# Kernel tuning notes

Hardware: AMD Instinct MI355X
Metric: run time of the kernel (lower is better)

## Reference

```python
import jax, jax.numpy as jnp
import numpy as np

B, S, D, H = 2, 2048, 1024, 16
DK = D // H

def setup_inputs() -> dict:
    key = jax.random.key(0)
    ks = jax.random.split(key, 8)
    inp = {
        "Q": jax.random.normal(ks[0], (B, S, D), dtype=jnp.float32),
        "K": jax.random.normal(ks[1], (B, S, D), dtype=jnp.float32),
        "V": jax.random.normal(ks[2], (B, S, D), dtype=jnp.float32),
        "mask": jax.random.randint(ks[3], (B, 1, S, S), 0, 2, dtype=jnp.int32),
        # nn.Linear weights, shape [out_features, in_features], no bias
        "Wq": jax.random.normal(ks[4], (D, D), dtype=jnp.float32) / np.sqrt(D),
        "Wk": jax.random.normal(ks[5], (D, D), dtype=jnp.float32) / np.sqrt(D),
        "Wv": jax.random.normal(ks[6], (D, D), dtype=jnp.float32) / np.sqrt(D),
        "Wo": jax.random.normal(ks[7], (D, D), dtype=jnp.float32) / np.sqrt(D),
    }
    return inp

def reference(Q, K, V, mask, Wq, Wk, Wv, Wo):
    b, s, d = Q.shape
    # projections: y = x @ W.T (torch nn.Linear convention)
    q = (Q @ Wq.T).reshape(b, s, H, DK).transpose(0, 2, 1, 3)  # [b,h,s,dk]
    k = (K @ Wk.T).reshape(b, -1, H, DK).transpose(0, 2, 1, 3)
    v = (V @ Wv.T).reshape(b, -1, H, DK).transpose(0, 2, 1, 3)
    score = jnp.einsum("bhqd,bhkd->bhqk", q, k) / jnp.sqrt(jnp.float32(DK))
    # faithful to source: masked positions get value 1e-9 BEFORE softmax
    score = jnp.where(mask == 0, jnp.float32(1e-9), score)
    attn = jax.nn.softmax(score, axis=-1)
    # dropout p=0.1 treated as eval-mode identity
    out = jnp.einsum("bhqk,bhkd->bhqd", attn, v)  # [b,h,s,dk]
    out = out.transpose(0, 2, 1, 3).reshape(b, s, d)
    return out @ Wo.T
```

## Files before the change

kernel.cpp:

```cpp
#include <hip/hip_runtime.h>

typedef unsigned short u16;
typedef unsigned char  u8;
typedef unsigned long long u64;
typedef __attribute__((ext_vector_type(8))) short bf16x8;
typedef __attribute__((ext_vector_type(4))) float f32x4;

constexpr int B_  = 2;
constexpr int S_  = 2048;
constexpr int D_  = 1024;
constexpr int H_  = 16;
constexpr int DK_ = 64;
constexpr int NROW = B_ * S_;
constexpr size_t QSZ  = (size_t)B_ * H_ * S_ * DK_;
constexpr size_t XBSZ = (size_t)NROW * D_;
constexpr size_t WBSZ = (size_t)D_ * D_;
constexpr size_t MSZ  = (size_t)B_ * S_ * S_;
constexpr size_t MPKB = MSZ / 8;

__device__ __forceinline__ u16 f2bf(float f) {
    union { float f; unsigned u; } c; c.f = f;
    unsigned r = c.u + 0x7fffu + ((c.u >> 16) & 1u);
    return (u16)(r >> 16);
}
__device__ __forceinline__ unsigned pack2(float a, float b) {
    return (unsigned)f2bf(a) | ((unsigned)f2bf(b) << 16);
}
__device__ __forceinline__ unsigned cvt_pk_bf16(float a, float b) {
    unsigned r;
    asm("v_cvt_pk_bf16_f32 %0, %1, %2" : "=v"(r) : "v"(a), "v"(b));
    return r;
}

__device__ __forceinline__ void gl_lds16(const u16* g, u16* l) {
    __builtin_amdgcn_global_load_lds(
        (const __attribute__((address_space(1))) void*)g,
        (__attribute__((address_space(3))) void*)l, 16, 0, 0);
}

__global__ __launch_bounds__(256)
void cvt7m(const float* __restrict__ s0, const float* __restrict__ s1,
           const float* __restrict__ s2, const float* __restrict__ s3,
           const float* __restrict__ s4, const float* __restrict__ s5,
           const float* __restrict__ s6, const int* __restrict__ mk,
           u16* __restrict__ d0, u16* __restrict__ d1, u16* __restrict__ d2,
           u16* __restrict__ d3, u16* __restrict__ d4, u16* __restrict__ d5,
           u16* __restrict__ d6, u8* __restrict__ mp)
{
    constexpr size_t XT = 3 * XBSZ;
    constexpr int NCF = (int)((3 * XBSZ + 4 * WBSZ) / 2048);
    constexpr int NCM = (int)(MSZ / 2048);

    for (int c = blockIdx.x; c < NCF + NCM; c += gridDim.x) {
        if (c < NCF) {
            const size_t base = (size_t)c * 2048;
            const float* s; u16* d; size_t off;
            if (base < XT) {
                const int a = (int)(base >> 22);
                off = base & (XBSZ - 1);
                s = (a == 0) ? s0 : (a == 1) ? s1 : s2;
                d = (a == 0) ? d0 : (a == 1) ? d1 : d2;
            } else {
                const size_t r = base - XT;
                const int a = (int)(r >> 20);
                off = r & (WBSZ - 1);
                s = (a == 0) ? s3 : (a == 1) ? s4 : (a == 2) ? s5 : s6;
                d = (a == 0) ? d3 : (a == 1) ? d4 : (a == 2) ? d5 : d6;
            }
            const size_t e = off + (size_t)threadIdx.x * 8;
            const float4 x0 = *(const float4*)(s + e);
            const float4 x1 = *(const float4*)(s + e + 4);
            uint4 p;
            p.x = pack2(x0.x, x0.y); p.y = pack2(x0.z, x0.w);
            p.z = pack2(x1.x, x1.y); p.w = pack2(x1.z, x1.w);
            *(uint4*)(d + e) = p;
        } else {
            const size_t e = (size_t)(c - NCF) * 2048 + (size_t)threadIdx.x * 8;
            const int4 x0 = *(const int4*)(mk + e);
            const int4 x1 = *(const int4*)(mk + e + 4);
            unsigned bv = (unsigned)(x0.x != 0)        | ((unsigned)(x0.y != 0) << 1)
                        | ((unsigned)(x0.z != 0) << 2) | ((unsigned)(x0.w != 0) << 3)
                        | ((unsigned)(x1.x != 0) << 4) | ((unsigned)(x1.y != 0) << 5)
                        | ((unsigned)(x1.z != 0) << 6) | ((unsigned)(x1.w != 0) << 7);
            mp[e >> 3] = (u8)bv;
        }
    }
}

__global__ __launch_bounds__(256, 3)
void qkv_gemm(const u16* __restrict__ Xq, const u16* __restrict__ Xk,
              const u16* __restrict__ Xv,
              const u16* __restrict__ Wq, const u16* __restrict__ Wk,
              const u16* __restrict__ Wv,
              u16* __restrict__ Yq, u16* __restrict__ Yk, u16* __restrict__ Yv)
{
    __shared__ u16 As[2 * 128 * 32];
    __shared__ u16 Bs[2 * 128 * 32];

    const int z = blockIdx.z;
    const u16* X = (z == 0) ? Xq : (z == 1) ? Xk : Xv;
    const u16* W = (z == 0) ? Wq : (z == 1) ? Wk : Wv;
    u16*       Y = (z == 0) ? Yq : (z == 1) ? Yk : Yv;
    const float osc = (z == 0) ? 0.125f : 1.0f;

    const int tid  = threadIdx.x;
    const int lane = tid & 63;
    const int w    = tid >> 6;
    const int quad = lane >> 4;
    const int lq   = lane & 15;
    const int wm   = (w & 1) << 6;
    const int wn   = (w >> 1) << 6;

    const int m0 = blockIdx.x << 7;
    const int n0 = blockIdx.y << 7;

    const int srow = tid >> 2;
    const int scol = (tid & 3) << 3;
    const u16* ga0 = X + (size_t)(m0 + srow) * D_ + scol;
    const u16* ga1 = ga0 + (size_t)64 * D_;
    const u16* gb0 = W + (size_t)(n0 + srow) * D_ + scol;
    const u16* gb1 = gb0 + (size_t)64 * D_;

    u16* la0 = As + (size_t)w * 512;
    u16* la1 = As + 2048 + (size_t)w * 512;
    u16* lb0 = Bs + (size_t)w * 512;
    u16* lb1 = Bs + 2048 + (size_t)w * 512;

    f32x4 acc[4][4];
#pragma unroll
    for (int i = 0; i < 4; ++i)
#pragma unroll
        for (int j = 0; j < 4; ++j) acc[i][j] = (f32x4){0.f, 0.f, 0.f, 0.f};

    for (int kt = 0; kt < D_; kt += 64) {
        __syncthreads();
        gl_lds16(ga0 + kt, la0);
        gl_lds16(ga1 + kt, la1);
        gl_lds16(gb0 + kt, lb0);
        gl_lds16(gb1 + kt, lb1);
        gl_lds16(ga0 + kt + 32, la0 + 4096);
        gl_lds16(ga1 + kt + 32, la1 + 4096);
        gl_lds16(gb0 + kt + 32, lb0 + 4096);
        gl_lds16(gb1 + kt + 32, lb1 + 4096);
        __syncthreads();

#pragma unroll
        for (int kk = 0; kk < 2; ++kk) {
            bf16x8 af[4], bf[4];
#pragma unroll
            for (int t = 0; t < 4; ++t) {
                af[t] = *(const bf16x8*)&As[(kk << 12) + (size_t)(wm + (t << 4) + lq) * 32 + (quad << 3)];
                bf[t] = *(const bf16x8*)&Bs[(kk << 12) + (size_t)(wn + (t << 4) + lq) * 32 + (quad << 3)];
            }
#pragma unroll
            for (int i = 0; i < 4; ++i)
#pragma unroll
                for (int j = 0; j < 4; ++j)
                    acc[i][j] = __builtin_amdgcn_mfma_f32_16x16x32_bf16(
                        af[i], bf[j], acc[i][j], 0, 0, 0);
        }
    }

#pragma unroll
    for (int i = 0; i < 4; ++i)
#pragma unroll
        for (int j = 0; j < 4; ++j)
#pragma unroll
            for (int r = 0; r < 4; ++r) {
                const int grow = m0 + wm + (i << 4) + (quad << 2) + r;
                const int of   = n0 + wn + (j << 4) + lq;
                const int b = grow >> 11, s = grow & (S_ - 1);
                const int h = of >> 6,    dk = of & 63;
                Y[(((size_t)(b * H_ + h)) * S_ + s) * DK_ + dk] =
                    f2bf(acc[i][j][r] * osc);
            }
}

__global__ __launch_bounds__(256, 4)
void out_gemm(const u16* __restrict__ X, const u16* __restrict__ W,
              float* __restrict__ Y)
{
    __shared__ u16 As[2 * 64 * 32];
    __shared__ u16 Bs[2 * 64 * 32];

    const int tid  = threadIdx.x;
    const int lane = tid & 63;
    const int w    = tid >> 6;
    const int quad = lane >> 4;
    const int lq   = lane & 15;
    const int wm   = (w & 1) << 5;
    const int wn   = (w >> 1) << 5;

    const int m0 = blockIdx.x << 6;
    const int n0 = blockIdx.y << 6;

    const int srow = tid >> 2;
    const int scol = (tid & 3) << 3;
    const u16* ga0 = X + (size_t)(m0 + srow) * D_ + scol;
    const u16* gb0 = W + (size_t)(n0 + srow) * D_ + scol;

    u16* la0 = As + (size_t)w * 512;
    u16* lb0 = Bs + (size_t)w * 512;

    f32x4 acc[2][2];
#pragma unroll
    for (int i = 0; i < 2; ++i)
#pragma unroll
        for (int j = 0; j < 2; ++j) acc[i][j] = (f32x4){0.f, 0.f, 0.f, 0.f};

    for (int kt = 0; kt < D_; kt += 64) {
        __syncthreads();
        gl_lds16(ga0 + kt, la0);
        gl_lds16(gb0 + kt, lb0);
        gl_lds16(ga0 + kt + 32, la0 + 2048);
        gl_lds16(gb0 + kt + 32, lb0 + 2048);
        __syncthreads();

#pragma unroll
        for (int kk = 0; kk < 2; ++kk) {
            bf16x8 af[2], bf[2];
#pragma unroll
            for (int t = 0; t < 2; ++t) {
                af[t] = *(const bf16x8*)&As[(kk << 11) + (size_t)(wm + (t << 4) + lq) * 32 + (quad << 3)];
                bf[t] = *(const bf16x8*)&Bs[(kk << 11) + (size_t)(wn + (t << 4) + lq) * 32 + (quad << 3)];
            }
#pragma unroll
            for (int i = 0; i < 2; ++i)
#pragma unroll
                for (int j = 0; j < 2; ++j)
                    acc[i][j] = __builtin_amdgcn_mfma_f32_16x16x32_bf16(
                        af[i], bf[j], acc[i][j], 0, 0, 0);
        }
    }

#pragma unroll
    for (int i = 0; i < 2; ++i)
#pragma unroll
        for (int j = 0; j < 2; ++j)
#pragma unroll
            for (int r = 0; r < 4; ++r) {
                const int grow = m0 + wm + (i << 4) + (quad << 2) + r;
                const int gcol = n0 + wn + (j << 4) + lq;
                Y[(size_t)grow * D_ + gcol] = acc[i][j][r];
            }
}

constexpr int AP = 72;

__global__ __launch_bounds__(256, 2)
void attn_mfma8(const u16* __restrict__ qb, const u16* __restrict__ kb,
                const u16* __restrict__ vb, const u8* __restrict__ mpk,
                u16* __restrict__ ctx)
{
    __shared__ u16 Qs[128][AP];
    __shared__ u16 Ks[64][AP];
    __shared__ u16 Vt[64][AP];
    __shared__ u16 Ps[128][AP];

    const int tid  = threadIdx.x;
    const int lane = tid & 63;
    const int w    = tid >> 6;
    const int quad = lane >> 4;
    const int lq   = lane & 15;
    const int w32  = w << 5;

    const int bid = (int)(blockIdx.x + gridDim.x * (blockIdx.y + gridDim.y * blockIdx.z));
    const int swz = (bid & 7) * 64 + (bid >> 3);
    const int q0 = (swz & 15) << 7;
    const int h  = (swz >> 4) & 15;
    const int b  = swz >> 8;

    const u16* qbh = qb + (((size_t)b * H_ + h) * S_ + q0) * DK_;
    const u16* kbh = kb + ((size_t)b * H_ + h) * S_ * DK_;
    const u16* vbh = vb + ((size_t)b * H_ + h) * S_ * DK_;

    {
        const int r = tid >> 1, c = (tid & 1) << 5;
#pragma unroll
        for (int u = 0; u < 4; ++u)
            *(uint4*)&Qs[r][c + (u << 3)] =
                *(const uint4*)&qbh[(size_t)r * DK_ + c + (u << 3)];
    }
    __syncthreads();
    bf16x8 aQ[2][2];
#pragma unroll
    for (int i = 0; i < 2; ++i) {
        aQ[i][0] = *(const bf16x8*)&Qs[w32 + (i << 4) + lq][quad << 3];
        aQ[i][1] = *(const bf16x8*)&Qs[w32 + (i << 4) + lq][32 + (quad << 3)];
    }

    f32x4 O[2][4];
    float lsum[2][4];
#pragma unroll
    for (int i = 0; i < 2; ++i)
#pragma unroll
        for (int t = 0; t < 4; ++t) O[i][t] = (f32x4){0.f, 0.f, 0.f, 0.f};
#pragma unroll
    for (int i = 0; i < 2; ++i)
#pragma unroll
        for (int r = 0; r < 4; ++r) lsum[i][r] = 0.f;

    const int ksr = tid >> 2, ksc = (tid & 3) << 4;
    const int vc  = tid & 15;
    const int vs  = (tid >> 4) & 1;
    const int vk0 = vc + (vs << 5);
    const int vdg = tid >> 5;
    const int vcol = (vc << 2) + (vs << 1);

    uint4 kr0, kr1, vr0, vr1;
    {
        kr0 = *(const uint4*)&kbh[(size_t)ksr * DK_ + ksc];
        kr1 = *(const uint4*)&kbh[(size_t)ksr * DK_ + ksc + 8];
        vr0 = *(const uint4*)&vbh[(size_t)vk0 * DK_ + (vdg << 3)];
        vr1 = *(const uint4*)&vbh[(size_t)(vk0 + 16) * DK_ + (vdg << 3)];
    }

    const int qrow0 = q0 + w32 + (quad << 2);
    const u8* mrow = mpk + (size_t)b * S_ * (S_ / 8) + (size_t)qrow0 * (S_ / 8);

    for (int k0 = 0; k0 < S_; k0 += 64) {
        u64 mw[2][4];
#pragma unroll
        for (int i = 0; i < 2; ++i)
#pragma unroll
            for (int r = 0; r < 4; ++r)
                mw[i][r] = *(const u64*)&mrow[(size_t)((i << 4) + r) * (S_ / 8) + (k0 >> 3)];

        __syncthreads();
        {
            *(uint4*)&Ks[ksr][ksc]     = kr0;
            *(uint4*)&Ks[ksr][ksc + 8] = kr1;
            const u16* a0 = (const u16*)&vr0;
            const u16* a1 = (const u16*)&vr1;
#pragma unroll
            for (int i = 0; i < 8; ++i)
                *(ushort2*)&Vt[(vdg << 3) + i][vcol] = (ushort2){a0[i], a1[i]};
        }
        __syncthreads();

        if (k0 + 64 < S_) {
            const size_t kb0 = (size_t)(k0 + 64 + ksr) * DK_ + ksc;
            kr0 = *(const uint4*)&kbh[kb0];
            kr1 = *(const uint4*)&kbh[kb0 + 8];
            const size_t vb0 = (size_t)(k0 + 64 + vk0) * DK_ + (vdg << 3);
            vr0 = *(const uint4*)&vbh[vb0];
            vr1 = *(const uint4*)&vbh[vb0 + (size_t)16 * DK_];
        }

        f32x4 st[2][4];
#pragma unroll
        for (int t = 0; t < 4; ++t) {
            const bf16x8 b0 = *(const bf16x8*)&Ks[(t << 4) + lq][quad << 3];
            const bf16x8 b1 = *(const bf16x8*)&Ks[(t << 4) + lq][32 + (quad << 3)];
#pragma unroll
            for (int i = 0; i < 2; ++i) {
                f32x4 c = {0.f, 0.f, 0.f, 0.f};
                c = __builtin_amdgcn_mfma_f32_16x16x32_bf16(aQ[i][0], b0, c, 0, 0, 0);
                c = __builtin_amdgcn_mfma_f32_16x16x32_bf16(aQ[i][1], b1, c, 0, 0, 0);
                st[i][t] = c;
            }
        }

#pragma unroll
        for (int i = 0; i < 2; ++i)
#pragma unroll
            for (int r = 0; r < 4; ++r) {
                const unsigned lo = (unsigned)mw[i][r];
                const unsigned hi = (unsigned)(mw[i][r] >> 32);
                float p0 = __expf(st[i][0][r]);
                float p1 = __expf(st[i][1][r]);
                float p2 = __expf(st[i][2][r]);
                float p3 = __expf(st[i][3][r]);
                p0 = ((lo >> lq) & 1u) ? p0 : 1.0f;
                p1 = ((lo >> (lq + 16)) & 1u) ? p1 : 1.0f;
                p2 = ((hi >> lq) & 1u) ? p2 : 1.0f;
                p3 = ((hi >> (lq + 16)) & 1u) ? p3 : 1.0f;
                lsum[i][r] += (p0 + p1) + (p2 + p3);
                uint2 pw;
                pw.x = cvt_pk_bf16(p0, p1);
                pw.y = cvt_pk_bf16(p2, p3);
                *(uint2*)&Ps[w32 + (i << 4) + (quad << 2) + r][lq << 2] = pw;
            }

        bf16x8 aP[2][2];
#pragma unroll
        for (int i = 0; i < 2; ++i) {
            aP[i][0] = *(const bf16x8*)&Ps[w32 + (i << 4) + lq][quad << 3];
            aP[i][1] = *(const bf16x8*)&Ps[w32 + (i << 4) + lq][32 + (quad << 3)];
        }
#pragma unroll
        for (int t = 0; t < 4; ++t) {
            const bf16x8 b0 = *(const bf16x8*)&Vt[(t << 4) + lq][quad << 3];
            const bf16x8 b1 = *(const bf16x8*)&Vt[(t << 4) + lq][32 + (quad << 3)];
#pragma unroll
            for (int i = 0; i < 2; ++i) {
                O[i][t] = __builtin_amdgcn_mfma_f32_16x16x32_bf16(aP[i][0], b0, O[i][t], 0, 0, 0);
                O[i][t] = __builtin_amdgcn_mfma_f32_16x16x32_bf16(aP[i][1], b1, O[i][t], 0, 0, 0);
            }
        }
    }

#pragma unroll
    for (int i = 0; i < 2; ++i)
#pragma unroll
        for (int r = 0; r < 4; ++r) {
#pragma unroll
            for (int off = 1; off < 16; off <<= 1)
                lsum[i][r] += __shfl_xor(lsum[i][r], off);
            lsum[i][r] = 1.0f / lsum[i][r];
        }

#pragma unroll
    for (int i = 0; i < 2; ++i)
#pragma unroll
        for (int t = 0; t < 4; ++t)
#pragma unroll
            for (int r = 0; r < 4; ++r) {
                const int row = qrow0 + (i << 4) + r;
                ctx[((size_t)b * S_ + row) * D_ + (h << 6) + (t << 4) + lq] =
                    f2bf(O[i][t][r] * lsum[i][r]);
            }
}

extern "C" void kernel_launch(void* const* d_in, const int* in_sizes, int n_in,
                              void* d_out, int out_size, void* d_ws, size_t ws_size,
                              hipStream_t stream)
{
    const float* Q    = (const float*)d_in[0];
    const float* K    = (const float*)d_in[1];
    const float* V    = (const float*)d_in[2];
    const int*   mask = (const int*)d_in[3];
    const float* Wq   = (const float*)d_in[4];
    const float* Wk   = (const float*)d_in[5];
    const float* Wv   = (const float*)d_in[6];
    const float* Wo   = (const float*)d_in[7];
    float* out = (float*)d_out;

    u16* xqb = (u16*)d_ws;
    u16* xkb = xqb + XBSZ;
    u16* xvb = xqb + 2 * XBSZ;
    u16* wqb = xqb + 3 * XBSZ;
    u16* wkb = wqb + WBSZ;
    u16* wvb = wqb + 2 * WBSZ;
    u16* wob = wqb + 3 * WBSZ;
    u16* qw  = wqb + 4 * WBSZ;
    u16* kw  = qw + QSZ;
    u16* vw  = qw + 2 * QSZ;
    u8*  mpk = (u8*)(qw + 3 * QSZ);
    u16* cx  = xqb;

    hipLaunchKernelGGL(cvt7m, dim3(2048), dim3(256), 0, stream,
                       Q, K, V, Wq, Wk, Wv, Wo, mask,
                       xqb, xkb, xvb, wqb, wkb, wvb, wob, mpk);
    hipLaunchKernelGGL(qkv_gemm, dim3(NROW / 128, D_ / 128, 3), dim3(256), 0, stream,
                       xqb, xkb, xvb, wqb, wkb, wvb, qw, kw, vw);
    hipLaunchKernelGGL(attn_mfma8, dim3(S_ / 128, H_, B_), dim3(256), 0, stream,
                       qw, kw, vw, mpk, cx);
    hipLaunchKernelGGL(out_gemm, dim3(NROW / 64, D_ / 64), dim3(256), 0, stream,
                       cx, wob, out);
}
```

Measured before the change: 252.0 us.

## Split attention block across 8 waves with warp-specialized K/V staging

```diff
diff --git a/kernel.cpp b/kernel.cpp
--- a/kernel.cpp
+++ b/kernel.cpp
@@ -247,22 +247,21 @@
 
 constexpr int AP = 72;
 
-__global__ __launch_bounds__(256, 2)
-void attn_mfma8(const u16* __restrict__ qb, const u16* __restrict__ kb,
+__global__ __launch_bounds__(512, 4)
+void attn_mfma9(const u16* __restrict__ qb, const u16* __restrict__ kb,
                 const u16* __restrict__ vb, const u8* __restrict__ mpk,
                 u16* __restrict__ ctx)
 {
-    __shared__ u16 Qs[128][AP];
-    __shared__ u16 Ks[64][AP];
-    __shared__ u16 Vt[64][AP];
-    __shared__ u16 Ps[128][AP];
+    __shared__ __align__(16) u16 Ks[64][AP];
+    __shared__ __align__(16) u16 Vt[64][AP];
+    __shared__ __align__(16) u16 Ps[128][AP];
 
     const int tid  = threadIdx.x;
     const int lane = tid & 63;
     const int w    = tid >> 6;
     const int quad = lane >> 4;
     const int lq   = lane & 15;
-    const int w32  = w << 5;
+    const int w16  = w << 4;
 
     const int bid = (int)(blockIdx.x + gridDim.x * (blockIdx.y + gridDim.y * blockIdx.z));
     const int swz = (bid & 7) * 64 + (bid >> 3);
@@ -274,62 +273,51 @@
     const u16* kbh = kb + ((size_t)b * H_ + h) * S_ * DK_;
     const u16* vbh = vb + ((size_t)b * H_ + h) * S_ * DK_;
 
+    bf16x8 aQ0, aQ1;
     {
-        const int r = tid >> 1, c = (tid & 1) << 5;
-#pragma unroll
-        for (int u = 0; u < 4; ++u)
-            *(uint4*)&Qs[r][c + (u << 3)] =
-                *(const uint4*)&qbh[(size_t)r * DK_ + c + (u << 3)];
-    }
-    __syncthreads();
-    bf16x8 aQ[2][2];
-#pragma unroll
-    for (int i = 0; i < 2; ++i) {
-        aQ[i][0] = *(const bf16x8*)&Qs[w32 + (i << 4) + lq][quad << 3];
-        aQ[i][1] = *(const bf16x8*)&Qs[w32 + (i << 4) + lq][32 + (quad << 3)];
-    }
-
-    f32x4 O[2][4];
-    float lsum[2][4];
-#pragma unroll
-    for (int i = 0; i < 2; ++i)
-#pragma unroll
-        for (int t = 0; t < 4; ++t) O[i][t] = (f32x4){0.f, 0.f, 0.f, 0.f};
-#pragma unroll
-    for (int i = 0; i < 2; ++i)
-#pragma unroll
-        for (int r = 0; r < 4; ++r) lsum[i][r] = 0.f;
+        const size_t qr = (size_t)(w16 + lq) * DK_;
+        aQ0 = *(const bf16x8*)&qbh[qr + (quad << 3)];
+        aQ1 = *(const bf16x8*)&qbh[qr + 32 + (quad << 3)];
+    }
+
+    f32x4 O[4];
+    float lsum[4];
+#pragma unroll
+    for (int t = 0; t < 4; ++t) O[t] = (f32x4){0.f, 0.f, 0.f, 0.f};
+#pragma unroll
+    for (int r = 0; r < 4; ++r) lsum[r] = 0.f;
 
     const int ksr = tid >> 2, ksc = (tid & 3) << 4;
-    const int vc  = tid & 15;
-    const int vs  = (tid >> 4) & 1;
+    const int t2  = tid - 256;
+    const int vc  = t2 & 15;
+    const int vs  = (t2 >> 4) & 1;
     const int vk0 = vc + (vs << 5);
-    const int vdg = tid >> 5;
+    const int vdg = t2 >> 5;
     const int vcol = (vc << 2) + (vs << 1);
 
     uint4 kr0, kr1, vr0, vr1;
-    {
+    if (w < 4) {
         kr0 = *(const uint4*)&kbh[(size_t)ksr * DK_ + ksc];
         kr1 = *(const uint4*)&kbh[(size_t)ksr * DK_ + ksc + 8];
+    } else {
         vr0 = *(const uint4*)&vbh[(size_t)vk0 * DK_ + (vdg << 3)];
         vr1 = *(const uint4*)&vbh[(size_t)(vk0 + 16) * DK_ + (vdg << 3)];
     }
 
-    const int qrow0 = q0 + w32 + (quad << 2);
+    const int qrow0 = q0 + w16 + (quad << 2);
     const u8* mrow = mpk + (size_t)b * S_ * (S_ / 8) + (size_t)qrow0 * (S_ / 8);
 
+    u64 mw[4], mwn[4];
+#pragma unroll
+    for (int r = 0; r < 4; ++r)
+        mw[r] = *(const u64*)&mrow[(size_t)r * (S_ / 8)];
+
     for (int k0 = 0; k0 < S_; k0 += 64) {
-        u64 mw[2][4];
-#pragma unroll
-        for (int i = 0; i < 2; ++i)
-#pragma unroll
-            for (int r = 0; r < 4; ++r)
-                mw[i][r] = *(const u64*)&mrow[(size_t)((i << 4) + r) * (S_ / 8) + (k0 >> 3)];
-
-        __syncthreads();
-        {
+        __syncthreads();
+        if (w < 4) {
             *(uint4*)&Ks[ksr][ksc]     = kr0;
             *(uint4*)&Ks[ksr][ksc + 8] = kr1;
+        } else {
             const u16* a0 = (const u16*)&vr0;
             const u16* a1 = (const u16*)&vr1;
 #pragma unroll
@@ -339,87 +327,87 @@
         __syncthreads();
 
         if (k0 + 64 < S_) {
-            const size_t kb0 = (size_t)(k0 + 64 + ksr) * DK_ + ksc;
-            kr0 = *(const uint4*)&kbh[kb0];
-            kr1 = *(const uint4*)&kbh[kb0 + 8];
-            const size_t vb0 = (size_t)(k0 + 64 + vk0) * DK_ + (vdg << 3);
-            vr0 = *(const uint4*)&vbh[vb0];
-            vr1 = *(const uint4*)&vbh[vb0 + (size_t)16 * DK_];
-        }
-
-        f32x4 st[2][4];
+            if (w < 4) {
+                const size_t kb0 = (size_t)(k0 + 64 + ksr) * DK_ + ksc;
+                kr0 = *(const uint4*)&kbh[kb0];
+                kr1 = *(const uint4*)&kbh[kb0 + 8];
+            } else {
+                const size_t vb0 = (size_t)(k0 + 64 + vk0) * DK_ + (vdg << 3);
+                vr0 = *(const uint4*)&vbh[vb0];
+                vr1 = *(const uint4*)&vbh[vb0 + (size_t)16 * DK_];
+            }
+#pragma unroll
+            for (int r = 0; r < 4; ++r)
+                mwn[r] = *(const u64*)&mrow[(size_t)r * (S_ / 8) + ((k0 + 64) >> 3)];
+        }
+
+        f32x4 st[4];
+        __builtin_amdgcn_s_setprio(1);
 #pragma unroll
         for (int t = 0; t < 4; ++t) {
             const bf16x8 b0 = *(const bf16x8*)&Ks[(t << 4) + lq][quad << 3];
             const bf16x8 b1 = *(const bf16x8*)&Ks[(t << 4) + lq][32 + (quad << 3)];
-#pragma unroll
-            for (int i = 0; i < 2; ++i) {
-                f32x4 c = {0.f, 0.f, 0.f, 0.f};
-                c = __builtin_amdgcn_mfma_f32_16x16x32_bf16(aQ[i][0], b0, c, 0, 0, 0);
-                c = __builtin_amdgcn_mfma_f32_16x16x32_bf16(aQ[i][1], b1, c, 0, 0, 0);
-                st[i][t] = c;
-            }
-        }
-
-#pragma unroll
-        for (int i = 0; i < 2; ++i)
-#pragma unroll
-            for (int r = 0; r < 4; ++r) {
-                const unsigned lo = (unsigned)mw[i][r];
-                const unsigned hi = (unsigned)(mw[i][r] >> 32);
-                float p0 = __expf(st[i][0][r]);
-                float p1 = __expf(st[i][1][r]);
-                float p2 = __expf(st[i][2][r]);
-                float p3 = __expf(st[i][3][r]);
-                p0 = ((lo >> lq) & 1u) ? p0 : 1.0f;
-                p1 = ((lo >> (lq + 16)) & 1u) ? p1 : 1.0f;
-                p2 = ((hi >> lq) & 1u) ? p2 : 1.0f;
-                p3 = ((hi >> (lq + 16)) & 1u) ? p3 : 1.0f;
-                lsum[i][r] += (p0 + p1) + (p2 + p3);
-                uint2 pw;
-                pw.x = cvt_pk_bf16(p0, p1);
-                pw.y = cvt_pk_bf16(p2, p3);
-                *(uint2*)&Ps[w32 + (i << 4) + (quad << 2) + r][lq << 2] = pw;
-            }
-
-        bf16x8 aP[2][2];
-#pragma unroll
-        for (int i = 0; i < 2; ++i) {
-            aP[i][0] = *(const bf16x8*)&Ps[w32 + (i << 4) + lq][quad << 3];
-            aP[i][1] = *(const bf16x8*)&Ps[w32 + (i << 4) + lq][32 + (quad << 3)];
-        }
+            f32x4 c = {0.f, 0.f, 0.f, 0.f};
+            c = __builtin_amdgcn_mfma_f32_16x16x32_bf16(aQ0, b0, c, 0, 0, 0);
+            c = __builtin_amdgcn_mfma_f32_16x16x32_bf16(aQ1, b1, c, 0, 0, 0);
+            st[t] = c;
+        }
+        __builtin_amdgcn_s_setprio(0);
+
+#pragma unroll
+        for (int r = 0; r < 4; ++r) {
+            const unsigned lo = (unsigned)mw[r];
+            const unsigned hi = (unsigned)(mw[r] >> 32);
+            float p0 = __expf(st[0][r]);
+            float p1 = __expf(st[1][r]);
+            float p2 = __expf(st[2][r]);
+            float p3 = __expf(st[3][r]);
+            p0 = ((lo >> lq) & 1u) ? p0 : 1.0f;
+            p1 = ((lo >> (lq + 16)) & 1u) ? p1 : 1.0f;
+            p2 = ((hi >> lq) & 1u) ? p2 : 1.0f;
+            p3 = ((hi >> (lq + 16)) & 1u) ? p3 : 1.0f;
+            lsum[r] += (p0 + p1) + (p2 + p3);
+            uint2 pw;
+            pw.x = cvt_pk_bf16(p0, p1);
+            pw.y = cvt_pk_bf16(p2, p3);
+            *(uint2*)&Ps[w16 + (quad << 2) + r][lq << 2] = pw;
+        }
+
+        bf16x8 aP0, aP1;
+        aP0 = *(const bf16x8*)&Ps[w16 + lq][quad << 3];
+        aP1 = *(const bf16x8*)&Ps[w16 + lq][32 + (quad << 3)];
+        __builtin_amdgcn_s_setprio(1);
 #pragma unroll
         for (int t = 0; t < 4; ++t) {
             const bf16x8 b0 = *(const bf16x8*)&Vt[(t << 4) + lq][quad << 3];
             const bf16x8 b1 = *(const bf16x8*)&Vt[(t << 4) + lq][32 + (quad << 3)];
-#pragma unroll
-            for (int i = 0; i < 2; ++i) {
-                O[i][t] = __builtin_amdgcn_mfma_f32_16x16x32_bf16(aP[i][0], b0, O[i][t], 0, 0, 0);
-                O[i][t] = __builtin_amdgcn_mfma_f32_16x16x32_bf16(aP[i][1], b1, O[i][t], 0, 0, 0);
-            }
-        }
-    }
-
-#pragma unroll
-    for (int i = 0; i < 2; ++i)
+            O[t] = __builtin_amdgcn_mfma_f32_16x16x32_bf16(aP0, b0, O[t], 0, 0, 0);
+            O[t] = __builtin_amdgcn_mfma_f32_16x16x32_bf16(aP1, b1, O[t], 0, 0, 0);
+        }
+        __builtin_amdgcn_s_setprio(0);
+
+        if (k0 + 64 < S_) {
+#pragma unroll
+            for (int r = 0; r < 4; ++r) mw[r] = mwn[r];
+        }
+    }
+
+#pragma unroll
+    for (int r = 0; r < 4; ++r) {
+#pragma unroll
+        for (int off = 1; off < 16; off <<= 1)
+            lsum[r] += __shfl_xor(lsum[r], off);
+        lsum[r] = 1.0f / lsum[r];
+    }
+
+#pragma unroll
+    for (int t = 0; t < 4; ++t)
 #pragma unroll
         for (int r = 0; r < 4; ++r) {
-#pragma unroll
-            for (int off = 1; off < 16; off <<= 1)
-                lsum[i][r] += __shfl_xor(lsum[i][r], off);
-            lsum[i][r] = 1.0f / lsum[i][r];
-        }
-
-#pragma unroll
-    for (int i = 0; i < 2; ++i)
-#pragma unroll
-        for (int t = 0; t < 4; ++t)
-#pragma unroll
-            for (int r = 0; r < 4; ++r) {
-                const int row = qrow0 + (i << 4) + r;
-                ctx[((size_t)b * S_ + row) * D_ + (h << 6) + (t << 4) + lq] =
-                    f2bf(O[i][t][r] * lsum[i][r]);
-            }
+            const int row = qrow0 + r;
+            ctx[((size_t)b * S_ + row) * D_ + (h << 6) + (t << 4) + lq] =
+                f2bf(O[t][r] * lsum[r]);
+        }
 }
 
 extern "C" void kernel_launch(void* const* d_in, const int* in_sizes, int n_in,
@@ -454,7 +442,7 @@
                        xqb, xkb, xvb, wqb, wkb, wvb, wob, mpk);
     hipLaunchKernelGGL(qkv_gemm, dim3(NROW / 128, D_ / 128, 3), dim3(256), 0, stream,
                        xqb, xkb, xvb, wqb, wkb, wvb, qw, kw, vw);
-    hipLaunchKernelGGL(attn_mfma8, dim3(S_ / 128, H_, B_), dim3(256), 0, stream,
+    hipLaunchKernelGGL(attn_mfma9, dim3(S_ / 128, H_, B_), dim3(512), 0, stream,
                        qw, kw, vw, mpk, cx);
     hipLaunchKernelGGL(out_gemm, dim3(NROW / 64, D_ / 64), dim3(256), 0, stream,
                        cx, wob, out);
```

New measurement: 253.0 us. Within noise of the previous version (+0.4%).

## Split attention key range in two and combine partial outputs in separate kernel

Applied to the files above, without the earlier changes.

```diff
diff --git a/kernel.cpp b/kernel.cpp
--- a/kernel.cpp
+++ b/kernel.cpp
@@ -17,6 +17,7 @@
 constexpr size_t WBSZ = (size_t)D_ * D_;
 constexpr size_t MSZ  = (size_t)B_ * S_ * S_;
 constexpr size_t MPKB = MSZ / 8;
+constexpr size_t NRH  = (size_t)B_ * H_ * S_;
 
 __device__ __forceinline__ u16 f2bf(float f) {
     union { float f; unsigned u; } c; c.f = f;
@@ -247,15 +248,15 @@
 
 constexpr int AP = 72;
 
-__global__ __launch_bounds__(256, 2)
-void attn_mfma8(const u16* __restrict__ qb, const u16* __restrict__ kb,
-                const u16* __restrict__ vb, const u8* __restrict__ mpk,
-                u16* __restrict__ ctx)
+__global__ __launch_bounds__(256, 4)
+void attn_mfma10(const u16* __restrict__ qb, const u16* __restrict__ kb,
+                 const u16* __restrict__ vb, const u8* __restrict__ mpk,
+                 float* __restrict__ opA, float* __restrict__ opB,
+                 float* __restrict__ lsA, float* __restrict__ lsB)
 {
-    __shared__ u16 Qs[128][AP];
-    __shared__ u16 Ks[64][AP];
-    __shared__ u16 Vt[64][AP];
-    __shared__ u16 Ps[128][AP];
+    __shared__ __align__(16) u16 Ks[64][AP];
+    __shared__ __align__(16) u16 Vt[64][AP];
+    __shared__ __align__(16) u16 Ps[128][AP];
 
     const int tid  = threadIdx.x;
     const int lane = tid & 63;
@@ -265,28 +266,22 @@
     const int w32  = w << 5;
 
     const int bid = (int)(blockIdx.x + gridDim.x * (blockIdx.y + gridDim.y * blockIdx.z));
-    const int swz = (bid & 7) * 64 + (bid >> 3);
-    const int q0 = (swz & 15) << 7;
-    const int h  = (swz >> 4) & 15;
-    const int b  = swz >> 8;
+    const int swz = (bid & 7) * 128 + (bid >> 3);
+    const int ks = swz & 1;
+    const int q0 = ((swz >> 1) & 15) << 7;
+    const int h  = (swz >> 5) & 15;
+    const int b  = swz >> 9;
 
     const u16* qbh = qb + (((size_t)b * H_ + h) * S_ + q0) * DK_;
-    const u16* kbh = kb + ((size_t)b * H_ + h) * S_ * DK_;
-    const u16* vbh = vb + ((size_t)b * H_ + h) * S_ * DK_;
-
-    {
-        const int r = tid >> 1, c = (tid & 1) << 5;
-#pragma unroll
-        for (int u = 0; u < 4; ++u)
-            *(uint4*)&Qs[r][c + (u << 3)] =
-                *(const uint4*)&qbh[(size_t)r * DK_ + c + (u << 3)];
-    }
-    __syncthreads();
+    const u16* kbh = kb + (((size_t)b * H_ + h) * S_ + (ks << 10)) * DK_;
+    const u16* vbh = vb + (((size_t)b * H_ + h) * S_ + (ks << 10)) * DK_;
+
     bf16x8 aQ[2][2];
 #pragma unroll
     for (int i = 0; i < 2; ++i) {
-        aQ[i][0] = *(const bf16x8*)&Qs[w32 + (i << 4) + lq][quad << 3];
-        aQ[i][1] = *(const bf16x8*)&Qs[w32 + (i << 4) + lq][32 + (quad << 3)];
+        const size_t qr = (size_t)(w32 + (i << 4) + lq) * DK_;
+        aQ[i][0] = *(const bf16x8*)&qbh[qr + (quad << 3)];
+        aQ[i][1] = *(const bf16x8*)&qbh[qr + 32 + (quad << 3)];
     }
 
     f32x4 O[2][4];
@@ -316,9 +311,10 @@
     }
 
     const int qrow0 = q0 + w32 + (quad << 2);
-    const u8* mrow = mpk + (size_t)b * S_ * (S_ / 8) + (size_t)qrow0 * (S_ / 8);
-
-    for (int k0 = 0; k0 < S_; k0 += 64) {
+    const u8* mrow = mpk + (size_t)b * S_ * (S_ / 8) + (size_t)qrow0 * (S_ / 8)
+                   + (ks << 7);
+
+    for (int k0 = 0; k0 < 1024; k0 += 64) {
         u64 mw[2][4];
 #pragma unroll
         for (int i = 0; i < 2; ++i)
@@ -338,7 +334,7 @@
         }
         __syncthreads();
 
-        if (k0 + 64 < S_) {
+        if (k0 + 64 < 1024) {
             const size_t kb0 = (size_t)(k0 + 64 + ksr) * DK_ + ksc;
             kr0 = *(const uint4*)&kbh[kb0];
             kr1 = *(const uint4*)&kbh[kb0 + 8];
@@ -348,6 +344,7 @@
         }
 
         f32x4 st[2][4];
+        __builtin_amdgcn_s_setprio(1);
 #pragma unroll
         for (int t = 0; t < 4; ++t) {
             const bf16x8 b0 = *(const bf16x8*)&Ks[(t << 4) + lq][quad << 3];
@@ -360,6 +357,7 @@
                 st[i][t] = c;
             }
         }
+        __builtin_amdgcn_s_setprio(0);
 
 #pragma unroll
         for (int i = 0; i < 2; ++i)
@@ -388,6 +386,7 @@
             aP[i][0] = *(const bf16x8*)&Ps[w32 + (i << 4) + lq][quad << 3];
             aP[i][1] = *(const bf16x8*)&Ps[w32 + (i << 4) + lq][32 + (quad << 3)];
         }
+        __builtin_amdgcn_s_setprio(1);
 #pragma unroll
         for (int t = 0; t < 4; ++t) {
             const bf16x8 b0 = *(const bf16x8*)&Vt[(t << 4) + lq][quad << 3];
@@ -398,6 +397,7 @@
                 O[i][t] = __builtin_amdgcn_mfma_f32_16x16x32_bf16(aP[i][1], b1, O[i][t], 0, 0, 0);
             }
         }
+        __builtin_amdgcn_s_setprio(0);
     }
 
 #pragma unroll
@@ -407,9 +407,11 @@
 #pragma unroll
             for (int off = 1; off < 16; off <<= 1)
                 lsum[i][r] += __shfl_xor(lsum[i][r], off);
-            lsum[i][r] = 1.0f / lsum[i][r];
-        }
-
+        }
+
+    float* op = ks ? opB : opA;
+    float* ls = ks ? lsB : lsA;
+    const size_t rbase = ((size_t)b * H_ + h) * S_;
 #pragma unroll
     for (int i = 0; i < 2; ++i)
 #pragma unroll
@@ -417,9 +419,44 @@
 #pragma unroll
             for (int r = 0; r < 4; ++r) {
                 const int row = qrow0 + (i << 4) + r;
-                ctx[((size_t)b * S_ + row) * D_ + (h << 6) + (t << 4) + lq] =
-                    f2bf(O[i][t][r] * lsum[i][r]);
-            }
+                op[(rbase + row) * DK_ + (t << 4) + lq] = O[i][t][r];
+            }
+    if (lq == 0) {
+#pragma unroll
+        for (int i = 0; i < 2; ++i)
+#pragma unroll
+            for (int r = 0; r < 4; ++r)
+                ls[rbase + qrow0 + (i << 4) + r] = lsum[i][r];
+    }
+}
+
+__global__ __launch_bounds__(256)
+void combine2(const float* __restrict__ opA, const float* __restrict__ opB,
+              const float* __restrict__ lsA, const float* __restrict__ lsB,
+              u16* __restrict__ ctx)
+{
+    const size_t t = (size_t)blockIdx.x * 256 + threadIdx.x;
+    const int row = (int)(t >> 3);
+    const int d0  = ((int)t & 7) << 3;
+    const float linv = 1.0f / (lsA[row] + lsB[row]);
+
+    const size_t base = (size_t)row * DK_ + d0;
+    const float4 a0 = *(const float4*)(opA + base);
+    const float4 a1 = *(const float4*)(opA + base + 4);
+    const float4 b0 = *(const float4*)(opB + base);
+    const float4 b1 = *(const float4*)(opB + base + 4);
+
+    ushort4 o0, o1;
+    o0.x = f2bf((a0.x + b0.x) * linv); o0.y = f2bf((a0.y + b0.y) * linv);
+    o0.z = f2bf((a0.z + b0.z) * linv); o0.w = f2bf((a0.w + b0.w) * linv);
+    o1.x = f2bf((a1.x + b1.x) * linv); o1.y = f2bf((a1.y + b1.y) * linv);
+    o1.z = f2bf((a1.z + b1.z) * linv); o1.w = f2bf((a1.w + b1.w) * linv);
+
+    const int bh = row >> 11, s = row & (S_ - 1);
+    const int b  = bh >> 4,   h = bh & 15;
+    u16* dst = ctx + ((size_t)b * S_ + s) * D_ + (h << 6) + d0;
+    *(ushort4*)(dst)     = o0;
+    *(ushort4*)(dst + 4) = o1;
 }
 
 extern "C" void kernel_launch(void* const* d_in, const int* in_sizes, int n_in,
@@ -447,15 +484,22 @@
     u16* kw  = qw + QSZ;
     u16* vw  = qw + 2 * QSZ;
     u8*  mpk = (u8*)(qw + 3 * QSZ);
-    u16* cx  = xqb;
+
+    float* opA = out;
+    float* opB = (float*)xqb;
+    float* lsA = (float*)xvb;
+    float* lsB = lsA + NRH;
+    u16*   cx  = qw;
 
     hipLaunchKernelGGL(cvt7m, dim3(2048), dim3(256), 0, stream,
                        Q, K, V, Wq, Wk, Wv, Wo, mask,
                        xqb, xkb, xvb, wqb, wkb, wvb, wob, mpk);
     hipLaunchKernelGGL(qkv_gemm, dim3(NROW / 128, D_ / 128, 3), dim3(256), 0, stream,
                        xqb, xkb, xvb, wqb, wkb, wvb, qw, kw, vw);
-    hipLaunchKernelGGL(attn_mfma8, dim3(S_ / 128, H_, B_), dim3(256), 0, stream,
-                       qw, kw, vw, mpk, cx);
+    hipLaunchKernelGGL(attn_mfma10, dim3(32, H_, B_), dim3(256), 0, stream,
+                       qw, kw, vw, mpk, opA, opB, lsA, lsB);
+    hipLaunchKernelGGL(combine2, dim3((unsigned)(NRH * 8 / 256)), dim3(256), 0, stream,
+                       opA, opB, lsA, lsB, cx);
     hipLaunchKernelGGL(out_gemm, dim3(NROW / 64, D_ / 64), dim3(256), 0, stream,
                        cx, wob, out);
 }
```

Result: slower. 303.8 us (+20.6%).
